# Performance work log

Measured on AMD Instinct MI355X. Metric: run time of the kernel, lower is better.

Reference implementation:

```python
import jax, jax.numpy as jnp
import numpy as np

EPS = 1e-12

def _normalize(x, axis=-1):
    # matches torch F.normalize: x / max(||x||, eps)
    n = jnp.sqrt(jnp.sum(x * x, axis=axis, keepdims=True))
    return x / jnp.maximum(n, EPS)

def setup_inputs() -> dict:
    key = jax.random.key(0)
    k1, k2, k3, k4, k5 = jax.random.split(key, 5)
    B, D, N = 65536, 512, 64
    feature = jax.random.normal(k1, (B, D), dtype=jnp.float32)
    target = jax.random.randint(k2, (B, N), 0, 2, dtype=jnp.int32)
    W = jax.random.normal(k3, (N, 2, D), dtype=jnp.float32) * 0.05
    b = jax.random.normal(k4, (N, 2), dtype=jnp.float32) * 0.01
    u = jax.random.normal(k5, (N, 2), dtype=jnp.float32)
    return {"feature": feature, "target": target, "W": W, "b": b, "u": u}

def reference(feature, target, W, b, u):
    # spectral norm, one power iteration per head (torch default n_power_iterations=1)
    v = _normalize(jnp.einsum('nod,no->nd', W, u))      # [N, D]
    u1 = _normalize(jnp.einsum('nod,nd->no', W, v))      # [N, 2]
    # u, v are buffers (no grad through them in torch)
    u_s = jax.lax.stop_gradient(u1)
    v_s = jax.lax.stop_gradient(v)
    sigma = jnp.einsum('no,nod,nd->n', u_s, W, v_s)      # [N]
    W_sn = W / sigma[:, None, None]
    # dropout in eval mode = identity; fused batched matmul over all heads
    pred = jnp.einsum('bd,nod->bno', feature, W_sn) + b[None]   # [B, N, 2]
    output = jnp.argmax(pred, axis=2)                           # [B, N]
    # CrossEntropyLoss with soft targets: class dim is dim=1 (nclass), as in torch code
    onehot = jax.nn.one_hot(target, 2, dtype=jnp.float32)       # [B, N, 2]
    logp = jax.nn.log_softmax(pred, axis=1)                     # softmax over nclass dim
    loss = jnp.mean(-jnp.sum(onehot * logp, axis=1))            # mean over B and the 2-dim
    return pred, output, loss
```

## Files before the change

### kernel.cpp

```cpp
#include <hip/hip_runtime.h>
#include <math.h>

typedef __bf16 bf16x8 __attribute__((ext_vector_type(8)));
typedef float  f32x4  __attribute__((ext_vector_type(4)));

#define BROWS 65536
#define DIM   512
#define NHEAD 64
#define NCOL  128

#define PRED_SZ  ((size_t)BROWS * NCOL)
#define ARG_BASE PRED_SZ
#define LOSS_IDX (PRED_SZ + (size_t)BROWS * NHEAD)
#define BH_OFF   ARG_BASE
#define BL_OFF   (ARG_BASE + 32768)
#define PART_OFF (ARG_BASE + 1056 * (size_t)NHEAD)
#define FIX_ROWS 1088

__global__ __launch_bounds__(64) void spectral_kernel(
    const float* __restrict__ W, const float* __restrict__ u,
    __bf16* __restrict__ Bh, __bf16* __restrict__ Bl)
{
    int n = blockIdx.x;
    int lane = threadIdx.x;

    const float* W0 = W + (size_t)n * 2 * DIM;
    const float* W1 = W0 + DIM;
    float u0 = u[n * 2 + 0], u1v = u[n * 2 + 1];

    float w0[8], w1[8], vr[8];
    float ss = 0.f;
#pragma unroll
    for (int i = 0; i < 8; ++i) {
        int d = lane + 64 * i;
        w0[i] = W0[d]; w1[i] = W1[d];
        vr[i] = fmaf(w0[i], u0, w1[i] * u1v);
        ss = fmaf(vr[i], vr[i], ss);
    }
#pragma unroll
    for (int m = 32; m >= 1; m >>= 1) ss += __shfl_xor(ss, m, 64);
    float inv_n = 1.f / fmaxf(sqrtf(ss), 1e-12f);

    float s0 = 0.f, s1 = 0.f;
#pragma unroll
    for (int i = 0; i < 8; ++i) {
        float v = vr[i] * inv_n;
        s0 = fmaf(w0[i], v, s0);
        s1 = fmaf(w1[i], v, s1);
    }
#pragma unroll
    for (int m = 32; m >= 1; m >>= 1) {
        s0 += __shfl_xor(s0, m, 64);
        s1 += __shfl_xor(s1, m, 64);
    }
    float nu = sqrtf(fmaf(s0, s0, s1 * s1));
    float inv_nu = 1.f / fmaxf(nu, 1e-12f);
    float uu0 = s0 * inv_nu, uu1 = s1 * inv_nu;
    float sigma = fmaf(uu0, s0, uu1 * s1);
    float inv_sigma = 1.f / sigma;

#pragma unroll
    for (int i = 0; i < 8; ++i) {
        int d = lane + 64 * i;
        float x0 = w0[i] * inv_sigma;
        float x1 = w1[i] * inv_sigma;
        __bf16 h0 = (__bf16)x0;
        __bf16 h1 = (__bf16)x1;
        Bh[(size_t)(2 * n + 0) * DIM + d] = h0;
        Bh[(size_t)(2 * n + 1) * DIM + d] = h1;
        Bl[(size_t)(2 * n + 0) * DIM + d] = (__bf16)(x0 - (float)h0);
        Bl[(size_t)(2 * n + 1) * DIM + d] = (__bf16)(x1 - (float)h1);
    }
}

#define CVT8(H, L, F0, F1) {                                   \
    float _v; __bf16 _h;                                       \
    _v = (F0).x; _h = (__bf16)_v; H[0] = _h; L[0] = (__bf16)(_v - (float)_h); \
    _v = (F0).y; _h = (__bf16)_v; H[1] = _h; L[1] = (__bf16)(_v - (float)_h); \
    _v = (F0).z; _h = (__bf16)_v; H[2] = _h; L[2] = (__bf16)(_v - (float)_h); \
    _v = (F0).w; _h = (__bf16)_v; H[3] = _h; L[3] = (__bf16)(_v - (float)_h); \
    _v = (F1).x; _h = (__bf16)_v; H[4] = _h; L[4] = (__bf16)(_v - (float)_h); \
    _v = (F1).y; _h = (__bf16)_v; H[5] = _h; L[5] = (__bf16)(_v - (float)_h); \
    _v = (F1).z; _h = (__bf16)_v; H[6] = _h; L[6] = (__bf16)(_v - (float)_h); \
    _v = (F1).w; _h = (__bf16)_v; H[7] = _h; L[7] = (__bf16)(_v - (float)_h); }

__global__ __launch_bounds__(256) void gemm_fused(
    const float* __restrict__ A, const int* __restrict__ target,
    const __bf16* __restrict__ Bh, const __bf16* __restrict__ Bl,
    const float* __restrict__ bias,
    float* __restrict__ pred, float* __restrict__ outArg,
    float* __restrict__ partials)
{
    int tid  = threadIdx.x;
    int wave = tid >> 6;
    int lane = tid & 63;
    int q = lane >> 4;
    int c = lane & 15;
    int rowBase = blockIdx.x * 128 + wave * 32;

    f32x4 acc[2][8] = {};

    const float*  a0p = A  + (size_t)(rowBase + c) * DIM + q * 8;
    const float*  a1p = a0p + (size_t)16 * DIM;
    const __bf16* bhp = Bh + (size_t)c * DIM + q * 8;
    const __bf16* blp = Bl + (size_t)c * DIM + q * 8;

#pragma unroll 2
    for (int s = 0; s < 16; ++s) {
        int k0 = s * 32;
        float4 x0 = *(const float4*)(a0p + k0);
        float4 x1 = *(const float4*)(a0p + k0 + 4);
        float4 y0 = *(const float4*)(a1p + k0);
        float4 y1 = *(const float4*)(a1p + k0 + 4);
        bf16x8 a0h, a0l, a1h, a1l;
        CVT8(a0h, a0l, x0, x1);
        CVT8(a1h, a1l, y0, y1);
#pragma unroll
        for (int nt = 0; nt < 8; ++nt) {
            bf16x8 bh = *(const bf16x8*)(bhp + (size_t)nt * 16 * DIM + k0);
            bf16x8 bl = *(const bf16x8*)(blp + (size_t)nt * 16 * DIM + k0);
            acc[0][nt] = __builtin_amdgcn_mfma_f32_16x16x32_bf16(a0h, bh, acc[0][nt], 0, 0, 0);
            acc[0][nt] = __builtin_amdgcn_mfma_f32_16x16x32_bf16(a0l, bh, acc[0][nt], 0, 0, 0);
            acc[0][nt] = __builtin_amdgcn_mfma_f32_16x16x32_bf16(a0h, bl, acc[0][nt], 0, 0, 0);
            acc[1][nt] = __builtin_amdgcn_mfma_f32_16x16x32_bf16(a1h, bh, acc[1][nt], 0, 0, 0);
            acc[1][nt] = __builtin_amdgcn_mfma_f32_16x16x32_bf16(a1l, bh, acc[1][nt], 0, 0, 0);
            acc[1][nt] = __builtin_amdgcn_mfma_f32_16x16x32_bf16(a1h, bl, acc[1][nt], 0, 0, 0);
        }
    }

    float bv[8];
#pragma unroll
    for (int nt = 0; nt < 8; ++nt) bv[nt] = bias[nt * 16 + c];

    float lp = 0.f;
#pragma unroll
    for (int mt = 0; mt < 2; ++mt) {
#pragma unroll
        for (int reg = 0; reg < 4; ++reg) {
            int row = rowBase + mt * 16 + q * 4 + reg;
            float p[8];
#pragma unroll
            for (int nt = 0; nt < 8; ++nt) p[nt] = acc[mt][nt][reg] + bv[nt];
#pragma unroll
            for (int nt = 0; nt < 8; ++nt)
                pred[(size_t)row * NCOL + nt * 16 + c] = p[nt];

            float M = p[0];
#pragma unroll
            for (int nt = 1; nt < 8; ++nt) M = fmaxf(M, p[nt]);
            M = fmaxf(M, __shfl_xor(M, 2, 64));
            M = fmaxf(M, __shfl_xor(M, 4, 64));
            M = fmaxf(M, __shfl_xor(M, 8, 64));
            float Mx = __shfl_xor(M, 1, 64);

            float sE = 0.f;
#pragma unroll
            for (int nt = 0; nt < 8; ++nt) sE += expf(p[nt] - M);
            sE += __shfl_xor(sE, 2, 64);
            sE += __shfl_xor(sE, 4, 64);
            sE += __shfl_xor(sE, 8, 64);
            float sX = __shfl_xor(sE, 1, 64);

            float Lown = M + logf(sE);
            float Loth = Mx + logf(sX);
            float L0 = (c & 1) ? Loth : Lown;
            float L1 = (c & 1) ? Lown : Loth;

            float pn[8];
#pragma unroll
            for (int nt = 0; nt < 8; ++nt) pn[nt] = __shfl_xor(p[nt], 1, 64);

            if ((c & 1) == 0) {
                bool doA = (row >= FIX_ROWS);
                const int* trow = target + (size_t)row * NHEAD;
                float* arow = outArg + (size_t)row * NHEAD;
#pragma unroll
                for (int nt = 0; nt < 8; ++nt) {
                    int head = nt * 8 + (c >> 1);
                    int t = trow[head];
                    lp += t ? (L1 - pn[nt]) : (L0 - p[nt]);
                    if (doA) arow[head] = (pn[nt] > p[nt]) ? 1.f : 0.f;
                }
            }
        }
    }

#pragma unroll
    for (int m = 32; m >= 1; m >>= 1) lp += __shfl_xor(lp, m, 64);
    __shared__ float wsum[4];
    if (lane == 0) wsum[wave] = lp;
    __syncthreads();
    if (tid == 0)
        partials[blockIdx.x] = (wsum[0] + wsum[1]) + (wsum[2] + wsum[3]);
}

__global__ __launch_bounds__(256) void fixup_kernel(
    const float* __restrict__ pred, const float* __restrict__ partials,
    float* __restrict__ outArg, float* __restrict__ lossOut)
{
    int tid = threadIdx.x;
    if (blockIdx.x == 0) {
        __shared__ double red[256];
        red[tid] = (double)partials[2 * tid] + (double)partials[2 * tid + 1];
        __syncthreads();
        for (int m = 128; m >= 1; m >>= 1) {
            if (tid < m) red[tid] += red[tid + m];
            __syncthreads();
        }
        if (tid == 0) lossOut[0] = (float)(red[0] / 131072.0);
        __syncthreads();
        int row = 1056 + (tid >> 3);
        int hb = (tid & 7) * 8;
        const float* pr = pred + (size_t)row * NCOL;
        float* ar = outArg + (size_t)row * NHEAD;
#pragma unroll
        for (int h = 0; h < 8; ++h) {
            float a = pr[2 * (hb + h)], b = pr[2 * (hb + h) + 1];
            ar[hb + h] = (b > a) ? 1.f : 0.f;
        }
    } else {
        int row = (blockIdx.x - 1) * 16 + (tid >> 4);
        int hb = (tid & 15) * 4;
        const float* pr = pred + (size_t)row * NCOL;
        float* ar = outArg + (size_t)row * NHEAD;
#pragma unroll
        for (int h = 0; h < 4; ++h) {
            float a = pr[2 * (hb + h)], b = pr[2 * (hb + h) + 1];
            ar[hb + h] = (b > a) ? 1.f : 0.f;
        }
    }
}

extern "C" void kernel_launch(void* const* d_in, const int* in_sizes, int n_in,
                              void* d_out, int out_size, void* d_ws, size_t ws_size,
                              hipStream_t stream) {
    const float* feature = (const float*)d_in[0];
    const int*   target  = (const int*)d_in[1];
    const float* W       = (const float*)d_in[2];
    const float* bias    = (const float*)d_in[3];
    const float* u       = (const float*)d_in[4];

    float* out     = (float*)d_out;
    float* pred    = out;
    float* outArg  = out + ARG_BASE;
    float* lossOut = out + LOSS_IDX;
    __bf16* Bh     = (__bf16*)(out + BH_OFF);
    __bf16* Bl     = (__bf16*)(out + BL_OFF);
    float* partial = out + PART_OFF;

    spectral_kernel<<<NHEAD, 64, 0, stream>>>(W, u, Bh, Bl);
    gemm_fused<<<BROWS / 128, 256, 0, stream>>>(feature, target, Bh, Bl, bias,
                                                pred, outArg, partial);
    fixup_kernel<<<67, 256, 0, stream>>>(pred, partial, outArg, lossOut);
}
```

Measured before the change: 285.6 us.

## Stage pre-swizzled split-bf16 weights in LDS and halve rows per block

```diff
diff --git a/kernel.cpp b/kernel.cpp
--- a/kernel.cpp
+++ b/kernel.cpp
@@ -12,30 +12,39 @@
 #define PRED_SZ  ((size_t)BROWS * NCOL)
 #define ARG_BASE PRED_SZ
 #define LOSS_IDX (PRED_SZ + (size_t)BROWS * NHEAD)
-#define BH_OFF   ARG_BASE
-#define BL_OFF   (ARG_BASE + 32768)
+#define BF_OFF   ARG_BASE
 #define PART_OFF (ARG_BASE + 1056 * (size_t)NHEAD)
 #define FIX_ROWS 1088
 
+
 __global__ __launch_bounds__(64) void spectral_kernel(
     const float* __restrict__ W, const float* __restrict__ u,
-    __bf16* __restrict__ Bh, __bf16* __restrict__ Bl)
+    __bf16* __restrict__ Bfrag)
 {
     int n = blockIdx.x;
     int lane = threadIdx.x;
 
     const float* W0 = W + (size_t)n * 2 * DIM;
     const float* W1 = W0 + DIM;
-    float u0 = u[n * 2 + 0], u1v = u[n * 2 + 1];
+    float u0 = u[2 * n], u1v = u[2 * n + 1];
 
     float w0[8], w1[8], vr[8];
+    {
+        float4 a0 = *(const float4*)(W0 + lane * 8);
+        float4 a1 = *(const float4*)(W0 + lane * 8 + 4);
+        float4 b0 = *(const float4*)(W1 + lane * 8);
+        float4 b1 = *(const float4*)(W1 + lane * 8 + 4);
+        w0[0]=a0.x; w0[1]=a0.y; w0[2]=a0.z; w0[3]=a0.w;
+        w0[4]=a1.x; w0[5]=a1.y; w0[6]=a1.z; w0[7]=a1.w;
+        w1[0]=b0.x; w1[1]=b0.y; w1[2]=b0.z; w1[3]=b0.w;
+        w1[4]=b1.x; w1[5]=b1.y; w1[6]=b1.z; w1[7]=b1.w;
+    }
+
     float ss = 0.f;
 #pragma unroll
-    for (int i = 0; i < 8; ++i) {
-        int d = lane + 64 * i;
-        w0[i] = W0[d]; w1[i] = W1[d];
-        vr[i] = fmaf(w0[i], u0, w1[i] * u1v);
-        ss = fmaf(vr[i], vr[i], ss);
+    for (int j = 0; j < 8; ++j) {
+        vr[j] = fmaf(w0[j], u0, w1[j] * u1v);
+        ss = fmaf(vr[j], vr[j], ss);
     }
 #pragma unroll
     for (int m = 32; m >= 1; m >>= 1) ss += __shfl_xor(ss, m, 64);
@@ -43,10 +52,10 @@
 
     float s0 = 0.f, s1 = 0.f;
 #pragma unroll
-    for (int i = 0; i < 8; ++i) {
-        float v = vr[i] * inv_n;
-        s0 = fmaf(w0[i], v, s0);
-        s1 = fmaf(w1[i], v, s1);
+    for (int j = 0; j < 8; ++j) {
+        float v = vr[j] * inv_n;
+        s0 = fmaf(w0[j], v, s0);
+        s1 = fmaf(w1[j], v, s1);
     }
 #pragma unroll
     for (int m = 32; m >= 1; m >>= 1) {
@@ -55,21 +64,27 @@
     }
     float nu = sqrtf(fmaf(s0, s0, s1 * s1));
     float inv_nu = 1.f / fmaxf(nu, 1e-12f);
-    float uu0 = s0 * inv_nu, uu1 = s1 * inv_nu;
-    float sigma = fmaf(uu0, s0, uu1 * s1);
+    float sigma = fmaf(s0 * inv_nu, s0, (s1 * inv_nu) * s1);
     float inv_sigma = 1.f / sigma;
 
-#pragma unroll
-    for (int i = 0; i < 8; ++i) {
-        int d = lane + 64 * i;
-        float x0 = w0[i] * inv_sigma;
-        float x1 = w1[i] * inv_sigma;
-        __bf16 h0 = (__bf16)x0;
-        __bf16 h1 = (__bf16)x1;
-        Bh[(size_t)(2 * n + 0) * DIM + d] = h0;
-        Bh[(size_t)(2 * n + 1) * DIM + d] = h1;
-        Bl[(size_t)(2 * n + 0) * DIM + d] = (__bf16)(x0 - (float)h0);
-        Bl[(size_t)(2 * n + 1) * DIM + d] = (__bf16)(x1 - (float)h1);
+    int kc = lane >> 3;
+    int s  = (lane >> 2) & 1;
+    int q  = lane & 3;
+#pragma unroll
+    for (int o = 0; o < 2; ++o) {
+        int col = 2 * n + o;
+        int nt = col >> 4, cc = col & 15;
+        bf16x8 hi, lo;
+#pragma unroll
+        for (int j = 0; j < 8; ++j) {
+            float x = (o ? w1[j] : w0[j]) * inv_sigma;
+            __bf16 h = (__bf16)x;
+            hi[j] = h;
+            lo[j] = (__bf16)(x - (float)h);
+        }
+        size_t base = (size_t)kc * 16384 + (size_t)(q * 16 + cc) * 8;
+        *(bf16x8*)(Bfrag + base + (size_t)((0 * 8 + nt) * 2 + s) * 512) = hi;
+        *(bf16x8*)(Bfrag + base + (size_t)((1 * 8 + nt) * 2 + s) * 512) = lo;
     }
 }
 
@@ -84,48 +99,74 @@
     _v = (F1).z; _h = (__bf16)_v; H[6] = _h; L[6] = (__bf16)(_v - (float)_h); \
     _v = (F1).w; _h = (__bf16)_v; H[7] = _h; L[7] = (__bf16)(_v - (float)_h); }
 
-__global__ __launch_bounds__(256) void gemm_fused(
+__device__ __forceinline__ void gld_lds16(const __bf16* g, __bf16* l) {
+    __builtin_amdgcn_global_load_lds(
+        (const __attribute__((address_space(1))) void*)g,
+        (__attribute__((address_space(3))) void*)l, 16, 0, 0);
+}
+
+__global__ __launch_bounds__(256, 4) void gemm_fused(
     const float* __restrict__ A, const int* __restrict__ target,
-    const __bf16* __restrict__ Bh, const __bf16* __restrict__ Bl,
-    const float* __restrict__ bias,
+    const __bf16* __restrict__ Bfrag, const float* __restrict__ bias,
     float* __restrict__ pred, float* __restrict__ outArg,
     float* __restrict__ partials)
 {
+    __shared__ __bf16 Bs[16384];
+    __shared__ float wsum[4];
+
     int tid  = threadIdx.x;
     int wave = tid >> 6;
     int lane = tid & 63;
     int q = lane >> 4;
     int c = lane & 15;
-    int rowBase = blockIdx.x * 128 + wave * 32;
-
-    f32x4 acc[2][8] = {};
-
-    const float*  a0p = A  + (size_t)(rowBase + c) * DIM + q * 8;
-    const float*  a1p = a0p + (size_t)16 * DIM;
-    const __bf16* bhp = Bh + (size_t)c * DIM + q * 8;
-    const __bf16* blp = Bl + (size_t)c * DIM + q * 8;
-
-#pragma unroll 2
-    for (int s = 0; s < 16; ++s) {
-        int k0 = s * 32;
-        float4 x0 = *(const float4*)(a0p + k0);
-        float4 x1 = *(const float4*)(a0p + k0 + 4);
-        float4 y0 = *(const float4*)(a1p + k0);
-        float4 y1 = *(const float4*)(a1p + k0 + 4);
-        bf16x8 a0h, a0l, a1h, a1l;
-        CVT8(a0h, a0l, x0, x1);
-        CVT8(a1h, a1l, y0, y1);
+    int rowBase = blockIdx.x * 64 + wave * 16;
+
+    f32x4 acc[8] = {};
+
+    const float*  ap = A + (size_t)(rowBase + c) * DIM + q * 8;
+    const __bf16* gB = Bfrag + (size_t)(wave * 8) * 512 + lane * 8;
+    __bf16*       lB = Bs + (size_t)(wave * 8) * 512;
+
+    float4 xa = *(const float4*)(ap + 0);
+    float4 xb = *(const float4*)(ap + 4);
+    float4 ya = *(const float4*)(ap + 32);
+    float4 yb = *(const float4*)(ap + 36);
+
+    for (int kc = 0; kc < 8; ++kc) {
+#pragma unroll
+        for (int t = 0; t < 8; ++t)
+            gld_lds16(gB + (size_t)kc * 16384 + t * 512, lB + t * 512);
+
+        int nb = (kc < 7) ? (kc + 1) * 64 : 0;
+        float4 nxa = *(const float4*)(ap + nb);
+        float4 nxb = *(const float4*)(ap + nb + 4);
+        float4 nya = *(const float4*)(ap + nb + 32);
+        float4 nyb = *(const float4*)(ap + nb + 36);
+
+        __syncthreads();
+
+        bf16x8 ah, al;
+        CVT8(ah, al, xa, xb);
 #pragma unroll
         for (int nt = 0; nt < 8; ++nt) {
-            bf16x8 bh = *(const bf16x8*)(bhp + (size_t)nt * 16 * DIM + k0);
-            bf16x8 bl = *(const bf16x8*)(blp + (size_t)nt * 16 * DIM + k0);
-            acc[0][nt] = __builtin_amdgcn_mfma_f32_16x16x32_bf16(a0h, bh, acc[0][nt], 0, 0, 0);
-            acc[0][nt] = __builtin_amdgcn_mfma_f32_16x16x32_bf16(a0l, bh, acc[0][nt], 0, 0, 0);
-            acc[0][nt] = __builtin_amdgcn_mfma_f32_16x16x32_bf16(a0h, bl, acc[0][nt], 0, 0, 0);
-            acc[1][nt] = __builtin_amdgcn_mfma_f32_16x16x32_bf16(a1h, bh, acc[1][nt], 0, 0, 0);
-            acc[1][nt] = __builtin_amdgcn_mfma_f32_16x16x32_bf16(a1l, bh, acc[1][nt], 0, 0, 0);
-            acc[1][nt] = __builtin_amdgcn_mfma_f32_16x16x32_bf16(a1h, bl, acc[1][nt], 0, 0, 0);
-        }
+            bf16x8 bh = *(const bf16x8*)(Bs + (size_t)((nt * 2 + 0) * 512) + lane * 8);
+            bf16x8 bl = *(const bf16x8*)(Bs + (size_t)(((8 + nt) * 2 + 0) * 512) + lane * 8);
+            acc[nt] = __builtin_amdgcn_mfma_f32_16x16x32_bf16(ah, bh, acc[nt], 0, 0, 0);
+            acc[nt] = __builtin_amdgcn_mfma_f32_16x16x32_bf16(al, bh, acc[nt], 0, 0, 0);
+            acc[nt] = __builtin_amdgcn_mfma_f32_16x16x32_bf16(ah, bl, acc[nt], 0, 0, 0);
+        }
+        CVT8(ah, al, ya, yb);
+#pragma unroll
+        for (int nt = 0; nt < 8; ++nt) {
+            bf16x8 bh = *(const bf16x8*)(Bs + (size_t)((nt * 2 + 1) * 512) + lane * 8);
+            bf16x8 bl = *(const bf16x8*)(Bs + (size_t)(((8 + nt) * 2 + 1) * 512) + lane * 8);
+            acc[nt] = __builtin_amdgcn_mfma_f32_16x16x32_bf16(ah, bh, acc[nt], 0, 0, 0);
+            acc[nt] = __builtin_amdgcn_mfma_f32_16x16x32_bf16(al, bh, acc[nt], 0, 0, 0);
+            acc[nt] = __builtin_amdgcn_mfma_f32_16x16x32_bf16(ah, bl, acc[nt], 0, 0, 0);
+        }
+        __syncthreads();
+
+        xa = nxa; xb = nxb; ya = nya; yb = nyb;
     }
 
     float bv[8];
@@ -133,61 +174,57 @@
     for (int nt = 0; nt < 8; ++nt) bv[nt] = bias[nt * 16 + c];
 
     float lp = 0.f;
-#pragma unroll
-    for (int mt = 0; mt < 2; ++mt) {
-#pragma unroll
-        for (int reg = 0; reg < 4; ++reg) {
-            int row = rowBase + mt * 16 + q * 4 + reg;
-            float p[8];
-#pragma unroll
-            for (int nt = 0; nt < 8; ++nt) p[nt] = acc[mt][nt][reg] + bv[nt];
-#pragma unroll
-            for (int nt = 0; nt < 8; ++nt)
-                pred[(size_t)row * NCOL + nt * 16 + c] = p[nt];
-
-            float M = p[0];
-#pragma unroll
-            for (int nt = 1; nt < 8; ++nt) M = fmaxf(M, p[nt]);
-            M = fmaxf(M, __shfl_xor(M, 2, 64));
-            M = fmaxf(M, __shfl_xor(M, 4, 64));
-            M = fmaxf(M, __shfl_xor(M, 8, 64));
-            float Mx = __shfl_xor(M, 1, 64);
-
-            float sE = 0.f;
-#pragma unroll
-            for (int nt = 0; nt < 8; ++nt) sE += expf(p[nt] - M);
-            sE += __shfl_xor(sE, 2, 64);
-            sE += __shfl_xor(sE, 4, 64);
-            sE += __shfl_xor(sE, 8, 64);
-            float sX = __shfl_xor(sE, 1, 64);
-
-            float Lown = M + logf(sE);
-            float Loth = Mx + logf(sX);
-            float L0 = (c & 1) ? Loth : Lown;
-            float L1 = (c & 1) ? Lown : Loth;
-
-            float pn[8];
-#pragma unroll
-            for (int nt = 0; nt < 8; ++nt) pn[nt] = __shfl_xor(p[nt], 1, 64);
-
-            if ((c & 1) == 0) {
-                bool doA = (row >= FIX_ROWS);
-                const int* trow = target + (size_t)row * NHEAD;
-                float* arow = outArg + (size_t)row * NHEAD;
-#pragma unroll
-                for (int nt = 0; nt < 8; ++nt) {
-                    int head = nt * 8 + (c >> 1);
-                    int t = trow[head];
-                    lp += t ? (L1 - pn[nt]) : (L0 - p[nt]);
-                    if (doA) arow[head] = (pn[nt] > p[nt]) ? 1.f : 0.f;
-                }
+    bool doA = (rowBase >= FIX_ROWS);
+#pragma unroll
+    for (int reg = 0; reg < 4; ++reg) {
+        int row = rowBase + q * 4 + reg;
+        float p[8];
+#pragma unroll
+        for (int nt = 0; nt < 8; ++nt) p[nt] = acc[nt][reg] + bv[nt];
+#pragma unroll
+        for (int nt = 0; nt < 8; ++nt)
+            pred[(size_t)row * NCOL + nt * 16 + c] = p[nt];
+
+        float M = p[0];
+#pragma unroll
+        for (int nt = 1; nt < 8; ++nt) M = fmaxf(M, p[nt]);
+        M = fmaxf(M, __shfl_xor(M, 2, 64));
+        M = fmaxf(M, __shfl_xor(M, 4, 64));
+        M = fmaxf(M, __shfl_xor(M, 8, 64));
+        float Mx = __shfl_xor(M, 1, 64);
+
+        float sE = 0.f;
+#pragma unroll
+        for (int nt = 0; nt < 8; ++nt) sE += expf(p[nt] - M);
+        sE += __shfl_xor(sE, 2, 64);
+        sE += __shfl_xor(sE, 4, 64);
+        sE += __shfl_xor(sE, 8, 64);
+        float sX = __shfl_xor(sE, 1, 64);
+
+        float Lown = M + logf(sE);
+        float Loth = Mx + logf(sX);
+        float L0 = (c & 1) ? Loth : Lown;
+        float L1 = (c & 1) ? Lown : Loth;
+
+        float pn[8];
+#pragma unroll
+        for (int nt = 0; nt < 8; ++nt) pn[nt] = __shfl_xor(p[nt], 1, 64);
+
+        if ((c & 1) == 0) {
+            const int* trow = target + (size_t)row * NHEAD;
+            float* arow = outArg + (size_t)row * NHEAD;
+#pragma unroll
+            for (int nt = 0; nt < 8; ++nt) {
+                int head = nt * 8 + (c >> 1);
+                int t = trow[head];
+                lp += t ? (L1 - pn[nt]) : (L0 - p[nt]);
+                if (doA) arow[head] = (pn[nt] > p[nt]) ? 1.f : 0.f;
             }
         }
     }
 
 #pragma unroll
     for (int m = 32; m >= 1; m >>= 1) lp += __shfl_xor(lp, m, 64);
-    __shared__ float wsum[4];
     if (lane == 0) wsum[wave] = lp;
     __syncthreads();
     if (tid == 0)
@@ -201,7 +238,10 @@
     int tid = threadIdx.x;
     if (blockIdx.x == 0) {
         __shared__ double red[256];
-        red[tid] = (double)partials[2 * tid] + (double)partials[2 * tid + 1];
+        double s = 0.0;
+#pragma unroll
+        for (int i = 0; i < 4; ++i) s += (double)partials[tid * 4 + i];
+        red[tid] = s;
         __syncthreads();
         for (int m = 128; m >= 1; m >>= 1) {
             if (tid < m) red[tid] += red[tid + m];
@@ -244,12 +284,11 @@
     float* pred    = out;
     float* outArg  = out + ARG_BASE;
     float* lossOut = out + LOSS_IDX;
-    __bf16* Bh     = (__bf16*)(out + BH_OFF);
-    __bf16* Bl     = (__bf16*)(out + BL_OFF);
+    __bf16* Bfrag  = (__bf16*)(out + BF_OFF);
     float* partial = out + PART_OFF;
 
-    spectral_kernel<<<NHEAD, 64, 0, stream>>>(W, u, Bh, Bl);
-    gemm_fused<<<BROWS / 128, 256, 0, stream>>>(feature, target, Bh, Bl, bias,
-                                                pred, outArg, partial);
+    spectral_kernel<<<NHEAD, 64, 0, stream>>>(W, u, Bfrag);
+    gemm_fused<<<BROWS / 64, 256, 0, stream>>>(feature, target, Bfrag, bias,
+                                               pred, outArg, partial);
     fixup_kernel<<<67, 256, 0, stream>>>(pred, partial, outArg, lossOut);
 }
```

Measured after the change: 242.4 us. -15.1%, faster.
